# Performance work log

Hardware: AMD Instinct MI355X
Metric: run time of the kernel (lower is better)

The kernel has to match this reference:

```python
import jax, jax.numpy as jnp
import numpy as np

C_CH, S_DIM, H_DIM, RANK = 256, 16, 128, 8


def setup_inputs() -> dict:
    key = jax.random.key(0)
    k = jax.random.split(key, 6)
    x = jax.random.normal(k[0], (1, C_CH, S_DIM, H_DIM, H_DIM), dtype=jnp.float32)
    # Conv1d(kernel=1, bias=False) weights per rank; kaiming-ish fan_out scaling
    W1 = jax.random.normal(k[1], (RANK, C_CH, C_CH), jnp.float32) * np.sqrt(2.0 / C_CH)
    W2 = jax.random.normal(k[2], (RANK, S_DIM, S_DIM), jnp.float32) * np.sqrt(2.0 / S_DIM)
    W3 = jax.random.normal(k[3], (RANK, H_DIM, H_DIM), jnp.float32) * np.sqrt(2.0 / H_DIM)
    W4 = jax.random.normal(k[4], (RANK, H_DIM, H_DIM), jnp.float32) * np.sqrt(2.0 / H_DIM)
    lam = jnp.ones((RANK,), dtype=jnp.float32)
    return {"x": x, "W1": W1, "W2": W2, "W3": W3, "W4": W4, "lam": lam}


def reference(x, W1, W2, W3, W4, lam):
    # x: (1, c, s, w, h); AdaptiveAvgPool3d(1) on permuted views == global means
    Cv = x.mean(axis=(0, 2, 3, 4))  # (c,)  channel pooling
    Sv = x.mean(axis=(0, 1, 3, 4))  # (s,)
    Hv = x.mean(axis=(0, 1, 2, 3))  # (h,)  last spatial dim
    Wv = x.mean(axis=(0, 1, 2, 4))  # (w,)

    # original detaches softmax(lam) and always uses index 0
    lam_sm = jax.lax.stop_gradient(jax.nn.softmax(lam))
    coef = lam_sm[0]

    # per-rank 1x1 conv + sigmoid == sigmoid(W @ v), batched over rank
    cf = jax.nn.sigmoid(jnp.einsum('rij,j->ri', W1, Cv))  # (r, c)
    sf = jax.nn.sigmoid(jnp.einsum('rij,j->ri', W2, Sv))  # (r, s)
    hf = jax.nn.sigmoid(jnp.einsum('rij,j->ri', W3, Hv))  # (r, h)
    wf = jax.nn.sigmoid(jnp.einsum('rij,j->ri', W4, Wv))  # (r, w)

    # chained bmm with ps=1 == rank-1 outer product, summed over rank
    tensor1 = coef * jnp.einsum('rc,rs,rh,rw->cshw', cf, sf, hf, wf)
    tensor1 = tensor1[None]  # (1, c, s, h, w) matching x layout

    return jnp.concatenate([x, jax.nn.relu(x * tensor1)], axis=1)
```

## Files before the change

### kernel.cpp

```cpp
#include <hip/hip_runtime.h>

typedef float f32x4 __attribute__((ext_vector_type(4)));
typedef unsigned short u16x4 __attribute__((ext_vector_type(4)));

#define C_CH 256
#define S_DIM 16
#define HW 128
#define RANK 8
#define NCOPY 16

#define OFF_PC 0
#define OFF_PS 4096
#define OFF_PI 4352
#define OFF_PJ 6400
#define OFF_CF 8448
#define OFF_SF 10496
#define OFF_HF 10624
#define OFF_WF 11648
#define OFF_BF 16384

#define BF_WS_BYTES ((size_t)65536 + (size_t)67108864 * 2)

__device__ __forceinline__ unsigned short bf16rne(float f) {
    unsigned u = __float_as_uint(f);
    return (unsigned short)((u + 0x7FFFu + ((u >> 16) & 1u)) >> 16);
}

__global__ __launch_bounds__(256) void k_init(float* __restrict__ ws) {
    int idx = blockIdx.x * 256 + threadIdx.x;
    if (idx < OFF_CF) ws[idx] = 0.f;
}

template <bool WBF>
__global__ __launch_bounds__(256) void k_reduce(const float* __restrict__ x,
                                                float* __restrict__ out,
                                                float* __restrict__ ws) {
    int b = blockIdx.x;
    int c = b >> 2;
    int s0 = (b & 3) * 4;
    int t = threadIdx.x;
    int lane = t & 31;
    int rg = t >> 5;
    int j0 = lane * 4;

    u16x4* bfp = reinterpret_cast<u16x4*>(
        reinterpret_cast<unsigned short*>(ws + OFF_BF));

    float colacc[4] = {0.f, 0.f, 0.f, 0.f};
    float rowacc[16] = {0.f};
    float tot[4] = {0.f, 0.f, 0.f, 0.f};

    for (int q = 0; q < 4; ++q) {
        size_t slab = (size_t)(b * 4 + q) * 16384;
        const f32x4* xs = reinterpret_cast<const f32x4*>(x + slab);
        f32x4* o1 = reinterpret_cast<f32x4*>(out + slab);
        u16x4* bf = bfp + (slab >> 2);
#pragma unroll
        for (int k = 0; k < 16; ++k) {
            f32x4 v = __builtin_nontemporal_load(&xs[k * 256 + t]);
            __builtin_nontemporal_store(v, &o1[k * 256 + t]);
            if (WBF) {
                u16x4 hv;
                hv.x = bf16rne(v.x);
                hv.y = bf16rne(v.y);
                hv.z = bf16rne(v.z);
                hv.w = bf16rne(v.w);
                bf[k * 256 + t] = hv;
            }
            colacc[0] += v.x; colacc[1] += v.y;
            colacc[2] += v.z; colacc[3] += v.w;
            float s4 = (v.x + v.y) + (v.z + v.w);
            rowacc[k] += s4;
            tot[q] += s4;
        }
    }

    __shared__ float ldsr[128 * 33];
    __shared__ float ldsc[128 * 9];
    __shared__ float ldst[4][4];

#pragma unroll
    for (int k = 0; k < 16; ++k) ldsr[(k * 8 + rg) * 33 + lane] = rowacc[k];
#pragma unroll
    for (int jj = 0; jj < 4; ++jj) ldsc[(j0 + jj) * 9 + rg] = colacc[jj];
#pragma unroll
    for (int q = 0; q < 4; ++q) {
        float v = tot[q];
        for (int d = 32; d > 0; d >>= 1) v += __shfl_down(v, d, 64);
        if ((t & 63) == 0) ldst[t >> 6][q] = v;
    }
    __syncthreads();

    int copy = b & (NCOPY - 1);
    if (t < 128) {
        float rsum = 0.f;
#pragma unroll
        for (int l = 0; l < 32; ++l) rsum += ldsr[t * 33 + l];
        atomicAdd(&ws[OFF_PI + copy * 128 + t], rsum);
    } else {
        int j = t - 128;
        float csum = 0.f;
#pragma unroll
        for (int g = 0; g < 8; ++g) csum += ldsc[j * 9 + g];
        atomicAdd(&ws[OFF_PJ + copy * 128 + j], csum);
    }
    if (t < 4) {
        float sv = ldst[0][t] + ldst[1][t] + ldst[2][t] + ldst[3][t];
        atomicAdd(&ws[OFF_PS + copy * 16 + s0 + t], sv);
    }
    if (t == 8) {
        float cv = 0.f;
#pragma unroll
        for (int w = 0; w < 4; ++w)
#pragma unroll
            for (int q = 0; q < 4; ++q) cv += ldst[w][q];
        atomicAdd(&ws[OFF_PC + copy * 256 + c], cv);
    }
}

__global__ __launch_bounds__(256) void k_factors(const float* __restrict__ W1,
                                                 const float* __restrict__ W2,
                                                 const float* __restrict__ W3,
                                                 const float* __restrict__ W4,
                                                 const float* __restrict__ lam,
                                                 float* __restrict__ ws) {
    __shared__ float mC[256], mS[16], mW[128], mH[128];
    int t = threadIdx.x;
    for (int idx = t; idx < 528; idx += 256) {
        float acc = 0.f;
        if (idx < 256) {
            for (int cp = 0; cp < NCOPY; ++cp) acc += ws[OFF_PC + cp * 256 + idx];
            mC[idx] = acc * (1.f / (S_DIM * 16384.f));
        } else if (idx < 272) {
            int q = idx - 256;
            for (int cp = 0; cp < NCOPY; ++cp) acc += ws[OFF_PS + cp * 16 + q];
            mS[q] = acc * (1.f / (C_CH * 16384.f));
        } else if (idx < 400) {
            int q = idx - 272;
            for (int cp = 0; cp < NCOPY; ++cp) acc += ws[OFF_PI + cp * 128 + q];
            mW[q] = acc * (1.f / (C_CH * S_DIM * 128.f));
        } else {
            int q = idx - 400;
            for (int cp = 0; cp < NCOPY; ++cp) acc += ws[OFF_PJ + cp * 128 + q];
            mH[q] = acc * (1.f / (C_CH * S_DIM * 128.f));
        }
    }
    __syncthreads();

    float m = lam[0];
    for (int r = 1; r < RANK; ++r) m = fmaxf(m, lam[r]);
    float den = 0.f;
    for (int r = 0; r < RANK; ++r) den += expf(lam[r] - m);
    float coef = expf(lam[0] - m) / den;

    int rid = blockIdx.x * 256 + t;
    if (rid < 2048) {
        int r = rid >> 8, i = rid & 255;
        const float* w = W1 + r * 65536 + i * 256;
        float d = 0.f;
        for (int k = 0; k < 256; ++k) d += w[k] * mC[k];
        ws[OFF_CF + rid] = coef / (1.f + expf(-d));
    } else if (rid < 2176) {
        int q = rid - 2048;
        int r = q >> 4, i = q & 15;
        const float* w = W2 + r * 256 + i * 16;
        float d = 0.f;
        for (int k = 0; k < 16; ++k) d += w[k] * mS[k];
        ws[OFF_SF + q] = 1.f / (1.f + expf(-d));
    } else if (rid < 3200) {
        int q = rid - 2176;
        int r = q >> 7, i = q & 127;
        const float* w = W3 + r * 16384 + i * 128;
        float d = 0.f;
        for (int k = 0; k < 128; ++k) d += w[k] * mH[k];
        ws[OFF_HF + q] = 1.f / (1.f + expf(-d));
    } else if (rid < 4224) {
        int q = rid - 3200;
        int r = q >> 7, i = q & 127;
        const float* w = W4 + r * 16384 + i * 128;
        float d = 0.f;
        for (int k = 0; k < 128; ++k) d += w[k] * mW[k];
        ws[OFF_WF + q] = 1.f / (1.f + expf(-d));
    }
}

__global__ __launch_bounds__(256) void k_output_bf(const float* __restrict__ ws,
                                                   float* __restrict__ out) {
    int b = blockIdx.x;
    int c = b >> 4, s = b & 15;
    int t = threadIdx.x;

    __shared__ float hb[128 * 8];
    __shared__ float wb[128 * 8];

    const float* cf = ws + OFF_CF;
    const float* sf = ws + OFF_SF;
    const float* hf = ws + OFF_HF;
    const float* wf = ws + OFF_WF;

    for (int idx = t; idx < 1024; idx += 256) {
        int r = idx & 7, p = idx >> 3;
        hb[idx] = hf[r * 128 + p];
        wb[idx] = cf[r * 256 + c] * sf[r * 16 + s] * wf[r * 128 + p];
    }
    __syncthreads();

    int j0 = (t & 31) * 4, rg = t >> 5;
    float wreg[4][8];
#pragma unroll
    for (int jj = 0; jj < 4; ++jj)
#pragma unroll
        for (int r = 0; r < 8; ++r) wreg[jj][r] = wb[(j0 + jj) * 8 + r];

    const u16x4* bf = reinterpret_cast<const u16x4*>(
        reinterpret_cast<const unsigned short*>(ws + OFF_BF));
    size_t slab4 = (size_t)b * 4096;
    f32x4* o2 = reinterpret_cast<f32x4*>(out + (size_t)67108864 + (size_t)b * 16384);

    for (int k = 0; k < 16; ++k) {
        int i = k * 8 + rg;
        int vidx = i * 32 + (t & 31);
        u16x4 hv = bf[slab4 + vidx];
        f32x4 v;
        v.x = __uint_as_float((unsigned)hv.x << 16);
        v.y = __uint_as_float((unsigned)hv.y << 16);
        v.z = __uint_as_float((unsigned)hv.z << 16);
        v.w = __uint_as_float((unsigned)hv.w << 16);
        float h[8];
#pragma unroll
        for (int r = 0; r < 8; ++r) h[r] = hb[i * 8 + r];
        float t0 = 0.f, t1 = 0.f, t2 = 0.f, t3 = 0.f;
#pragma unroll
        for (int r = 0; r < 8; ++r) {
            t0 += h[r] * wreg[0][r];
            t1 += h[r] * wreg[1][r];
            t2 += h[r] * wreg[2][r];
            t3 += h[r] * wreg[3][r];
        }
        f32x4 y;
        y.x = fmaxf(v.x * t0, 0.f);
        y.y = fmaxf(v.y * t1, 0.f);
        y.z = fmaxf(v.z * t2, 0.f);
        y.w = fmaxf(v.w * t3, 0.f);
        __builtin_nontemporal_store(y, &o2[vidx]);
    }
}

__global__ __launch_bounds__(256) void k_output_fp(const float* __restrict__ x,
                                                   const float* __restrict__ ws,
                                                   float* __restrict__ out) {
    int b = blockIdx.x;
    int c = b >> 4, s = b & 15;
    int t = threadIdx.x;

    __shared__ float hb[128 * 8];
    __shared__ float wb[128 * 8];

    const float* cf = ws + OFF_CF;
    const float* sf = ws + OFF_SF;
    const float* hf = ws + OFF_HF;
    const float* wf = ws + OFF_WF;

    for (int idx = t; idx < 1024; idx += 256) {
        int r = idx & 7, p = idx >> 3;
        hb[idx] = hf[r * 128 + p];
        wb[idx] = cf[r * 256 + c] * sf[r * 16 + s] * wf[r * 128 + p];
    }
    __syncthreads();

    int j0 = (t & 31) * 4, rg = t >> 5;
    float wreg[4][8];
#pragma unroll
    for (int jj = 0; jj < 4; ++jj)
#pragma unroll
        for (int r = 0; r < 8; ++r) wreg[jj][r] = wb[(j0 + jj) * 8 + r];

    size_t slab = (size_t)b * 16384;
    const f32x4* xs = reinterpret_cast<const f32x4*>(x + slab);
    f32x4* o2 = reinterpret_cast<f32x4*>(out + (size_t)67108864 + slab);

    for (int k = 0; k < 16; ++k) {
        int i = k * 8 + rg;
        int vidx = i * 32 + (t & 31);
        f32x4 v = xs[vidx];
        float h[8];
#pragma unroll
        for (int r = 0; r < 8; ++r) h[r] = hb[i * 8 + r];
        float t0 = 0.f, t1 = 0.f, t2 = 0.f, t3 = 0.f;
#pragma unroll
        for (int r = 0; r < 8; ++r) {
            t0 += h[r] * wreg[0][r];
            t1 += h[r] * wreg[1][r];
            t2 += h[r] * wreg[2][r];
            t3 += h[r] * wreg[3][r];
        }
        f32x4 y;
        y.x = fmaxf(v.x * t0, 0.f);
        y.y = fmaxf(v.y * t1, 0.f);
        y.z = fmaxf(v.z * t2, 0.f);
        y.w = fmaxf(v.w * t3, 0.f);
        __builtin_nontemporal_store(y, &o2[vidx]);
    }
}

extern "C" void kernel_launch(void* const* d_in, const int* in_sizes, int n_in,
                              void* d_out, int out_size, void* d_ws, size_t ws_size,
                              hipStream_t stream) {
    const float* x   = (const float*)d_in[0];
    const float* W1  = (const float*)d_in[1];
    const float* W2  = (const float*)d_in[2];
    const float* W3  = (const float*)d_in[3];
    const float* W4  = (const float*)d_in[4];
    const float* lam = (const float*)d_in[5];
    float* ws  = (float*)d_ws;
    float* out = (float*)d_out;

    bool use_bf = ws_size >= BF_WS_BYTES;

    k_init<<<33, 256, 0, stream>>>(ws);
    if (use_bf) {
        k_reduce<true><<<1024, 256, 0, stream>>>(x, out, ws);
        k_factors<<<17, 256, 0, stream>>>(W1, W2, W3, W4, lam, ws);
        k_output_bf<<<4096, 256, 0, stream>>>(ws, out);
    } else {
        k_reduce<false><<<1024, 256, 0, stream>>>(x, out, ws);
        k_factors<<<17, 256, 0, stream>>>(W1, W2, W3, W4, lam, ws);
        k_output_fp<<<4096, 256, 0, stream>>>(x, ws, out);
    }
}
```

Measured before the change: 193.2 us.

## Replace atomic partial reductions with per-block stores and drop init kernel

Each reduce block now writes its partial row, column, slice and channel sums to a dedicated workspace slot instead of atomically adding into 16 replicated copies. This removes the zero-init kernel launch and the atomic contention. In exchange the factors kernel must sum 1024 partials per entry (256 or 64 float4 loads per thread) serially in a single-block-sized stage, and the workspace requirement grows. The fp output path also switches its x read to a nontemporal load.

```diff
diff --git a/kernel.cpp b/kernel.cpp
--- a/kernel.cpp
+++ b/kernel.cpp
@@ -7,28 +7,22 @@
 #define S_DIM 16
 #define HW 128
 #define RANK 8
-#define NCOPY 16
-
-#define OFF_PC 0
-#define OFF_PS 4096
-#define OFF_PI 4352
-#define OFF_PJ 6400
-#define OFF_CF 8448
-#define OFF_SF 10496
-#define OFF_HF 10624
-#define OFF_WF 11648
-#define OFF_BF 16384
-
-#define BF_WS_BYTES ((size_t)65536 + (size_t)67108864 * 2)
+
+#define OFF_PI 0
+#define OFF_PJ 131072
+#define OFF_PS 262144
+#define OFF_PC 266240
+#define OFF_CF 267264
+#define OFF_SF 269312
+#define OFF_HF 269440
+#define OFF_WF 270464
+#define OFF_BF 524288
+
+#define BF_WS_BYTES ((size_t)2097152 + (size_t)67108864 * 2)
 
 __device__ __forceinline__ unsigned short bf16rne(float f) {
     unsigned u = __float_as_uint(f);
     return (unsigned short)((u + 0x7FFFu + ((u >> 16) & 1u)) >> 16);
-}
-
-__global__ __launch_bounds__(256) void k_init(float* __restrict__ ws) {
-    int idx = blockIdx.x * 256 + threadIdx.x;
-    if (idx < OFF_CF) ws[idx] = 0.f;
 }
 
 template <bool WBF>
@@ -36,8 +30,6 @@
                                                 float* __restrict__ out,
                                                 float* __restrict__ ws) {
     int b = blockIdx.x;
-    int c = b >> 2;
-    int s0 = (b & 3) * 4;
     int t = threadIdx.x;
     int lane = t & 31;
     int rg = t >> 5;
@@ -91,22 +83,21 @@
     }
     __syncthreads();
 
-    int copy = b & (NCOPY - 1);
     if (t < 128) {
         float rsum = 0.f;
 #pragma unroll
         for (int l = 0; l < 32; ++l) rsum += ldsr[t * 33 + l];
-        atomicAdd(&ws[OFF_PI + copy * 128 + t], rsum);
+        ws[OFF_PI + t * 1024 + b] = rsum;
     } else {
         int j = t - 128;
         float csum = 0.f;
 #pragma unroll
         for (int g = 0; g < 8; ++g) csum += ldsc[j * 9 + g];
-        atomicAdd(&ws[OFF_PJ + copy * 128 + j], csum);
+        ws[OFF_PJ + j * 1024 + b] = csum;
     }
     if (t < 4) {
         float sv = ldst[0][t] + ldst[1][t] + ldst[2][t] + ldst[3][t];
-        atomicAdd(&ws[OFF_PS + copy * 16 + s0 + t], sv);
+        ws[OFF_PS + ((b & 3) * 4 + t) * 256 + (b >> 2)] = sv;
     }
     if (t == 8) {
         float cv = 0.f;
@@ -114,7 +105,7 @@
         for (int w = 0; w < 4; ++w)
 #pragma unroll
             for (int q = 0; q < 4; ++q) cv += ldst[w][q];
-        atomicAdd(&ws[OFF_PC + copy * 256 + c], cv);
+        ws[OFF_PC + (b >> 2) * 4 + (b & 3)] = cv;
     }
 }
 
@@ -127,22 +118,38 @@
     __shared__ float mC[256], mS[16], mW[128], mH[128];
     int t = threadIdx.x;
     for (int idx = t; idx < 528; idx += 256) {
-        float acc = 0.f;
         if (idx < 256) {
-            for (int cp = 0; cp < NCOPY; ++cp) acc += ws[OFF_PC + cp * 256 + idx];
-            mC[idx] = acc * (1.f / (S_DIM * 16384.f));
+            const float* pc = ws + OFF_PC + idx * 4;
+            mC[idx] = (pc[0] + pc[1] + pc[2] + pc[3]) * (1.f / (S_DIM * 16384.f));
         } else if (idx < 272) {
-            int q = idx - 256;
-            for (int cp = 0; cp < NCOPY; ++cp) acc += ws[OFF_PS + cp * 16 + q];
-            mS[q] = acc * (1.f / (C_CH * 16384.f));
+            int s = idx - 256;
+            const f32x4* p = reinterpret_cast<const f32x4*>(ws + OFF_PS + s * 256);
+            float a = 0.f;
+            for (int k = 0; k < 64; ++k) {
+                f32x4 v = p[k];
+                a += (v.x + v.y) + (v.z + v.w);
+            }
+            mS[s] = a * (1.f / (C_CH * 16384.f));
         } else if (idx < 400) {
             int q = idx - 272;
-            for (int cp = 0; cp < NCOPY; ++cp) acc += ws[OFF_PI + cp * 128 + q];
-            mW[q] = acc * (1.f / (C_CH * S_DIM * 128.f));
+            const f32x4* p = reinterpret_cast<const f32x4*>(ws + OFF_PI + q * 1024);
+            float a0 = 0.f, a1 = 0.f;
+            for (int k = 0; k < 256; k += 2) {
+                f32x4 v0 = p[k], v1 = p[k + 1];
+                a0 += (v0.x + v0.y) + (v0.z + v0.w);
+                a1 += (v1.x + v1.y) + (v1.z + v1.w);
+            }
+            mW[q] = (a0 + a1) * (1.f / (C_CH * S_DIM * 128.f));
         } else {
             int q = idx - 400;
-            for (int cp = 0; cp < NCOPY; ++cp) acc += ws[OFF_PJ + cp * 128 + q];
-            mH[q] = acc * (1.f / (C_CH * S_DIM * 128.f));
+            const f32x4* p = reinterpret_cast<const f32x4*>(ws + OFF_PJ + q * 1024);
+            float a0 = 0.f, a1 = 0.f;
+            for (int k = 0; k < 256; k += 2) {
+                f32x4 v0 = p[k], v1 = p[k + 1];
+                a0 += (v0.x + v0.y) + (v0.z + v0.w);
+                a1 += (v1.x + v1.y) + (v1.z + v1.w);
+            }
+            mH[q] = (a0 + a1) * (1.f / (C_CH * S_DIM * 128.f));
         }
     }
     __syncthreads();
@@ -282,7 +289,7 @@
     for (int k = 0; k < 16; ++k) {
         int i = k * 8 + rg;
         int vidx = i * 32 + (t & 31);
-        f32x4 v = xs[vidx];
+        f32x4 v = __builtin_nontemporal_load(&xs[vidx]);
         float h[8];
 #pragma unroll
         for (int r = 0; r < 8; ++r) h[r] = hb[i * 8 + r];
@@ -317,7 +324,6 @@
 
     bool use_bf = ws_size >= BF_WS_BYTES;
 
-    k_init<<<33, 256, 0, stream>>>(ws);
     if (use_bf) {
         k_reduce<true><<<1024, 256, 0, stream>>>(x, out, ws);
         k_factors<<<17, 256, 0, stream>>>(W1, W2, W3, W4, lam, ws);
```

After: 235.8 us. 22.0% more time.
